# Kernel optimization log

Measured on AMD Instinct MI355X. Metric: run time of the kernel, lower is better.

Reference implementation:

```python
import jax, jax.numpy as jnp
import numpy as np

H = 8          # num_heads
SPARSITY = 0.1


def setup_inputs() -> dict:
    key = jax.random.key(0)
    ks = jax.random.split(key, 16)
    B, S, D = 2, 2048, 1024
    g2 = H * H  # 64, distill width
    std = 0.02
    inp = {
        "x":   jax.random.normal(ks[0], (B, S, D), dtype=jnp.float32),
        "Wq":  jax.random.normal(ks[1], (D, D)) * std, "bq": jnp.zeros((D,)),
        "Wk":  jax.random.normal(ks[2], (D, D)) * std, "bk": jnp.zeros((D,)),
        "Wv":  jax.random.normal(ks[3], (D, D)) * std, "bv": jnp.zeros((D,)),
        "Wo":  jax.random.normal(ks[4], (D, D)) * std, "bo": jnp.zeros((D,)),
        "Wd":  jax.random.normal(ks[5], (g2, g2)) * std, "bd": jnp.zeros((g2,)),
        "Wg":  jax.random.normal(ks[6], (g2, D)) * std,  "bg": jnp.zeros((g2,)),
        "Wgp": jax.random.normal(ks[7], (D, g2)) * std,  "bgp": jnp.zeros((D,)),
    }
    return inp


def reference(x, Wq, bq, Wk, bk, Wv, bv, Wo, bo, Wd, bd, Wg, bg, Wgp, bgp):
    B, S, D = x.shape
    Dh = D // H
    scale = Dh ** -0.5
    k = max(int(S * SPARSITY), 1)

    def heads(W, b):  # [B,S,D] -> [B,H,S,Dh]
        return (x @ W.T + b).reshape(B, S, H, Dh).transpose(0, 2, 1, 3)

    Q, K, V = heads(Wq, bq), heads(Wk, bk), heads(Wv, bv)

    scores = jnp.einsum("bhqd,bhkd->bhqk", Q, K) * scale       # [B,H,S,S]
    # per-row top-k threshold (k-th largest value of each query row)
    thr = jax.lax.top_k(scores, k)[0][..., k - 1:k]              # [B,H,S,1]
    masked = jnp.where(scores >= thr, scores, -jnp.inf)
    probs = jax.nn.softmax(masked, axis=-1)
    attn = jnp.einsum("bhqk,bhkd->bhqd", probs, V)               # [B,H,S,Dh]
    attn = attn.transpose(0, 2, 1, 3).reshape(B, S, D)           # [B,S,D]

    g2 = H * H
    distilled = (attn.reshape(-1, g2) @ Wd.T + bd).reshape(B, S, D)

    gate = jax.nn.sigmoid(x.mean(axis=1) @ Wg.T + bg)            # [B,g2]
    gate = (gate @ Wgp.T + bgp)[:, None, :]                      # [B,1,D]

    mixed = gate * distilled + (1.0 - gate) * attn
    return mixed @ Wo.T + bo
```

## Files before the change

kernel.cpp:

```cpp
#include <hip/hip_runtime.h>

typedef __attribute__((ext_vector_type(8))) short bf16x8;
typedef __attribute__((ext_vector_type(4))) float f32x4;
typedef __attribute__((ext_vector_type(4))) unsigned int u32x4;

#define DEVINL __device__ __forceinline__

DEVINL unsigned short f2bf(float f){
  unsigned int u = __float_as_uint(f);
  unsigned int r = (u + 0x7FFFu + ((u >> 16) & 1u)) >> 16;
  return (unsigned short)r;
}
DEVINL float bf2f(unsigned short h){ return __uint_as_float(((unsigned int)h) << 16); }
DEVINL unsigned int fkey(float f){
  unsigned int u = __float_as_uint(f);
  return (u & 0x80000000u) ? ~u : (u | 0x80000000u);
}
DEVINL float fkeyinv(unsigned int k){
  unsigned int u = (k & 0x80000000u) ? (k & 0x7FFFFFFFu) : ~k;
  return __uint_as_float(u);
}
DEVINL unsigned int cvtpk(float lo, float hi){
  unsigned int r;
  asm("v_cvt_pk_bf16_f32 %0, %1, %2" : "=v"(r) : "v"(lo), "v"(hi));
  return r;
}
DEVINL void gload16(void* lds, const void* g){
  __builtin_amdgcn_global_load_lds((const __attribute__((address_space(1))) void*)g,
                                   (__attribute__((address_space(3))) void*)lds, 16, 0, 0);
}

__global__ void prep_split_kernel(const float* __restrict__ src,
                                  unsigned short* __restrict__ hi,
                                  unsigned short* __restrict__ lo, int n){
  int i = blockIdx.x * 256 + threadIdx.x;
  if (i >= n) return;
  float f = src[i];
  unsigned short h = f2bf(f);
  hi[i] = h;
  if (lo) lo[i] = f2bf(f - bf2f(h));
}

template<bool SPLIT, int EPI>
__global__ __launch_bounds__(256) void gemm_kernel(
    const unsigned short* __restrict__ Ah, const unsigned short* __restrict__ Al,
    const unsigned short* __restrict__ Bh, const unsigned short* __restrict__ Bl,
    const float* __restrict__ bias0, const float* __restrict__ bias1, const float* __restrict__ bias2,
    unsigned short* __restrict__ qh, unsigned short* __restrict__ ql,
    unsigned short* __restrict__ kh, unsigned short* __restrict__ kl,
    unsigned short* __restrict__ vT, float* __restrict__ outf)
{
  const int K = 1024;
  __shared__ __align__(16) unsigned short sAh[128*32];
  __shared__ __align__(16) unsigned short sBh[128*32];
  __shared__ __align__(16) unsigned short sAl[SPLIT ? 128*32 : 8];
  __shared__ __align__(16) unsigned short sBl[SPLIT ? 128*32 : 8];

  const int tid = threadIdx.x;
  const int lane = tid & 63;
  const int w = tid >> 6;
  const int wr = w >> 1, wc = w & 1;
  const int l16 = lane & 15, lg = lane >> 4;
  const int bm = blockIdx.x, bn = blockIdx.y;

  const int srow = (lane >> 2);
  const int scol = (lane & 3) * 8;
  const int r0 = w * 32;

  f32x4 acc[4][4];
  #pragma unroll
  for (int i = 0; i < 4; i++)
    #pragma unroll
    for (int j = 0; j < 4; j++)
      acc[i][j] = (f32x4){0.f,0.f,0.f,0.f};

  for (int kt = 0; kt < K/32; ++kt){
    __syncthreads();
    #pragma unroll
    for (int cc = 0; cc < 2; cc++){
      const int rr = r0 + cc*16 + srow;
      const int lb = (r0 + cc*16) * 32;
      gload16(&sAh[lb], &Ah[(size_t)(bm*128 + rr)*K + kt*32 + scol]);
      gload16(&sBh[lb], &Bh[(size_t)(bn*128 + rr)*K + kt*32 + scol]);
      if constexpr (SPLIT){
        gload16(&sAl[lb], &Al[(size_t)(bm*128 + rr)*K + kt*32 + scol]);
        gload16(&sBl[lb], &Bl[(size_t)(bn*128 + rr)*K + kt*32 + scol]);
      }
    }
    __syncthreads();

    bf16x8 afh[4], afl[4], bfh[4], bfl[4];
    #pragma unroll
    for (int mi = 0; mi < 4; mi++){
      int off = (wr*64 + mi*16 + l16)*32 + lg*8;
      afh[mi] = *(const bf16x8*)&sAh[off];
      if constexpr (SPLIT) afl[mi] = *(const bf16x8*)&sAl[off];
    }
    #pragma unroll
    for (int ni = 0; ni < 4; ni++){
      int off = (wc*64 + ni*16 + l16)*32 + lg*8;
      bfh[ni] = *(const bf16x8*)&sBh[off];
      if constexpr (SPLIT) bfl[ni] = *(const bf16x8*)&sBl[off];
    }
    #pragma unroll
    for (int mi = 0; mi < 4; mi++)
      #pragma unroll
      for (int ni = 0; ni < 4; ni++){
        acc[mi][ni] = __builtin_amdgcn_mfma_f32_16x16x32_bf16(afh[mi], bfh[ni], acc[mi][ni], 0, 0, 0);
        if constexpr (SPLIT){
          acc[mi][ni] = __builtin_amdgcn_mfma_f32_16x16x32_bf16(afh[mi], bfl[ni], acc[mi][ni], 0, 0, 0);
          acc[mi][ni] = __builtin_amdgcn_mfma_f32_16x16x32_bf16(afl[mi], bfh[ni], acc[mi][ni], 0, 0, 0);
        }
      }
  }

  if constexpr (EPI == 0){
    const int wsel = (bn * 128) >> 10;
    const float* bias = (wsel == 0) ? bias0 : (wsel == 1) ? bias1 : bias2;
    #pragma unroll
    for (int mi = 0; mi < 4; mi++)
      #pragma unroll
      for (int ni = 0; ni < 4; ni++)
        #pragma unroll
        for (int i = 0; i < 4; i++){
          int m = bm*128 + wr*64 + mi*16 + lg*4 + i;
          int ng = bn*128 + wc*64 + ni*16 + l16;
          int n = ng & 1023;
          float v = acc[mi][ni][i] + bias[n];
          int b = m >> 11, s = m & 2047;
          int h = n >> 7, dh = n & 127;
          size_t base = (size_t)(b*8 + h)*262144;
          if (wsel == 2){
            size_t off = base + (size_t)(s>>5)*4096 + (dh>>4)*512
                       + (size_t)((((s>>3)&3)*16 + (dh&15))*8 + (s&7));
            vT[off] = f2bf(v);
          } else {
            size_t off = base + (size_t)(s>>4)*2048 + (dh>>5)*512
                       + (size_t)((((dh>>3)&3)*16 + (s&15))*8 + (dh&7));
            unsigned short hv = f2bf(v);
            if (wsel == 0){ qh[off] = hv; ql[off] = f2bf(v - bf2f(hv)); }
            else          { kh[off] = hv; kl[off] = f2bf(v - bf2f(hv)); }
          }
        }
  } else {
    #pragma unroll
    for (int mi = 0; mi < 4; mi++)
      #pragma unroll
      for (int ni = 0; ni < 4; ni++)
        #pragma unroll
        for (int i = 0; i < 4; i++){
          int m = bm*128 + wr*64 + mi*16 + lg*4 + i;
          int n = bn*128 + wc*64 + ni*16 + l16;
          outf[(size_t)m*1024 + n] = acc[mi][ni][i] + bias0[n];
        }
  }
}

__global__ __launch_bounds__(512, 4) void attn_kernel(
    const unsigned short* __restrict__ qh, const unsigned short* __restrict__ ql,
    const unsigned short* __restrict__ kh, const unsigned short* __restrict__ kl,
    const unsigned short* __restrict__ vT, float* __restrict__ attn_out)
{
  __shared__ __align__(16) float red[8][16][132];
  __shared__ float rpartm[8][16], rpartd[8][16];
  __shared__ unsigned int prefixv[16], kremv[16];
  unsigned int* hist = (unsigned int*)red;

  const int tid = threadIdx.x;
  const int lane = tid & 63;
  const int w = tid >> 6;
  const int l16 = lane & 15, lg = lane >> 4;
  const int swz = (blockIdx.x & 7) * 256 + (blockIdx.x >> 3);
  const int bh = swz >> 7, qb = swz & 127;
  const float scale = 0.08838834764831845f;

  const size_t base = (size_t)bh*262144;

  const size_t qpb = base + (size_t)qb*2048 + lane*8;
  bf16x8 aqh[4], aql[4];
  #pragma unroll
  for (int kk = 0; kk < 4; kk++){
    aqh[kk] = *(const bf16x8*)&qh[qpb + kk*512];
    aql[kk] = *(const bf16x8*)&ql[qpb + kk*512];
  }

  f32x4 acc[16];
  #pragma unroll
  for (int nt = 0; nt < 16; nt++){
    f32x4 a0 = (f32x4){0.f,0.f,0.f,0.f};
    f32x4 a1 = (f32x4){0.f,0.f,0.f,0.f};
    const size_t kb = base + (size_t)(w*16 + nt)*2048 + lane*8;
    __builtin_amdgcn_s_setprio(1);
    #pragma unroll
    for (int kk = 0; kk < 4; kk++){
      bf16x8 kbh = *(const bf16x8*)&kh[kb + kk*512];
      bf16x8 kbl = *(const bf16x8*)&kl[kb + kk*512];
      a0 = __builtin_amdgcn_mfma_f32_16x16x32_bf16(kbh, aqh[kk], a0, 0, 0, 0);
      a1 = __builtin_amdgcn_mfma_f32_16x16x32_bf16(kbh, aql[kk], a1, 0, 0, 0);
      a1 = __builtin_amdgcn_mfma_f32_16x16x32_bf16(kbl, aqh[kk], a1, 0, 0, 0);
    }
    __builtin_amdgcn_s_setprio(0);
    #pragma unroll
    for (int i = 0; i < 4; i++) acc[nt][i] = (a0[i] + a1[i]) * scale;
  }

  {
    float rm = -3.4e38f;
    #pragma unroll
    for (int nt = 0; nt < 16; nt++)
      #pragma unroll
      for (int i = 0; i < 4; i++) rm = fmaxf(rm, acc[nt][i]);
    rm = fmaxf(rm, __shfl_xor(rm, 16, 64));
    rm = fmaxf(rm, __shfl_xor(rm, 32, 64));
    if (lane < 16) rpartm[w][lane] = rm;
  }
  if (tid < 16){ prefixv[tid] = 0u; kremv[tid] = 204u; }

  #pragma unroll
  for (int nt = 0; nt < 16; nt++)
    #pragma unroll
    for (int i = 0; i < 4; i++)
      acc[nt][i] = __uint_as_float(fkey(acc[nt][i]));

  const int hco = (w >> 1) * (16*257);
  for (int pass = 3; pass >= 0; pass--){
    const int shift = pass*8;
    __syncthreads();
    for (int j = tid; j < 4*16*257; j += 512) hist[j] = 0u;
    __syncthreads();
    const unsigned int pf = prefixv[l16];
    const unsigned int mhi = (pass == 3) ? 0u : (0xFFFFFFFFu << (shift + 8));
    #pragma unroll
    for (int nt = 0; nt < 16; nt++)
      #pragma unroll
      for (int i = 0; i < 4; i++){
        unsigned int u = __float_as_uint(acc[nt][i]);
        if ((u & mhi) == pf)
          atomicAdd(&hist[hco + l16*257 + ((u >> shift) & 255u)], 1u);
      }
    __syncthreads();
    #pragma unroll
    for (int rr = 0; rr < 2; rr++){
      int r = w*2 + rr;
      unsigned int krem = kremv[r];
      unsigned int pfx  = prefixv[r];
      unsigned int cl[4], s4 = 0;
      #pragma unroll
      for (int t = 0; t < 4; t++){
        int idx = r*257 + 255 - 4*lane - t;
        cl[t] = hist[idx] + hist[16*257 + idx] + hist[2*16*257 + idx] + hist[3*16*257 + idx];
        s4 += cl[t];
      }
      unsigned int inc = s4;
      #pragma unroll
      for (int off = 1; off < 64; off <<= 1){
        unsigned int v = __shfl_up((int)inc, off, 64);
        if (lane >= off) inc += v;
      }
      unsigned int cb = inc - s4;
      #pragma unroll
      for (int t = 0; t < 4; t++){
        if (krem > cb && krem <= cb + cl[t]){
          int d = 255 - 4*lane - t;
          prefixv[r] = pfx | ((unsigned int)d << shift);
          kremv[r]   = krem - cb;
        }
        cb += cl[t];
      }
    }
  }
  __syncthreads();

  const unsigned int th = prefixv[l16];
  float rmax = rpartm[0][l16];
  #pragma unroll
  for (int w8 = 1; w8 < 8; w8++) rmax = fmaxf(rmax, rpartm[w8][l16]);
  const int src01 = ((lg & 1) << 5) + l16;
  const int src23 = src01 + 16;
  const size_t vb0 = base + (size_t)(w*8)*4096 + lane*8;
  float dn = 0.f;
  f32x4 pacc[8];
  #pragma unroll
  for (int dt = 0; dt < 8; dt++) pacc[dt] = (f32x4){0.f,0.f,0.f,0.f};
  #pragma unroll
  for (int t = 0; t < 8; t++){
    float p[8];
    #pragma unroll
    for (int j = 0; j < 4; j++){
      unsigned int u = __float_as_uint(acc[2*t][j]);
      p[j] = (u >= th) ? __expf(fkeyinv(u) - rmax) : 0.f;
    }
    #pragma unroll
    for (int j = 0; j < 4; j++){
      unsigned int u = __float_as_uint(acc[2*t+1][j]);
      p[4+j] = (u >= th) ? __expf(fkeyinv(u) - rmax) : 0.f;
    }
    unsigned int d0 = cvtpk(p[0], p[1]), d1 = cvtpk(p[2], p[3]);
    unsigned int d2 = cvtpk(p[4], p[5]), d3 = cvtpk(p[6], p[7]);
    dn += __uint_as_float(d0 << 16) + __uint_as_float(d0 & 0xFFFF0000u)
        + __uint_as_float(d1 << 16) + __uint_as_float(d1 & 0xFFFF0000u)
        + __uint_as_float(d2 << 16) + __uint_as_float(d2 & 0xFFFF0000u)
        + __uint_as_float(d3 << 16) + __uint_as_float(d3 & 0xFFFF0000u);
    unsigned int A0 = (unsigned int)__shfl((int)d0, src01, 64);
    unsigned int A1 = (unsigned int)__shfl((int)d1, src01, 64);
    unsigned int A2 = (unsigned int)__shfl((int)d0, src23, 64);
    unsigned int A3 = (unsigned int)__shfl((int)d1, src23, 64);
    unsigned int B0 = (unsigned int)__shfl((int)d2, src01, 64);
    unsigned int B1 = (unsigned int)__shfl((int)d3, src01, 64);
    unsigned int B2 = (unsigned int)__shfl((int)d2, src23, 64);
    unsigned int B3 = (unsigned int)__shfl((int)d3, src23, 64);
    u32x4 pdv = (lg < 2) ? (u32x4){A0, A1, A2, A3} : (u32x4){B0, B1, B2, B3};
    bf16x8 pa = __builtin_bit_cast(bf16x8, pdv);
    __builtin_amdgcn_s_setprio(1);
    #pragma unroll
    for (int dt = 0; dt < 8; dt++){
      bf16x8 bv = *(const bf16x8*)&vT[vb0 + (size_t)t*4096 + dt*512];
      pacc[dt] = __builtin_amdgcn_mfma_f32_16x16x32_bf16(pa, bv, pacc[dt], 0, 0, 0);
    }
    __builtin_amdgcn_s_setprio(0);
  }
  dn += __shfl_xor(dn, 16, 64);
  dn += __shfl_xor(dn, 32, 64);
  if (lane < 16) rpartd[w][lane] = dn;

  #pragma unroll
  for (int dt = 0; dt < 8; dt++)
    #pragma unroll
    for (int i = 0; i < 4; i++)
      red[w][lg*4 + i][dt*16 + l16] = pacc[dt][i];
  __syncthreads();

  {
    const int q = tid >> 5;
    const int c0 = (tid & 31) * 4;
    f32x4 s0 = (f32x4){0.f,0.f,0.f,0.f};
    #pragma unroll
    for (int w8 = 0; w8 < 8; w8++)
      s0 += *(const f32x4*)&red[w8][q][c0];
    float dnm = 0.f;
    #pragma unroll
    for (int w8 = 0; w8 < 8; w8++) dnm += rpartd[w8][q];
    const int b = bh >> 3, h = bh & 7;
    float* op = &attn_out[((size_t)b*2048 + qb*16 + q)*1024 + h*128 + c0];
    f32x4 o0;
    #pragma unroll
    for (int i = 0; i < 4; i++) o0[i] = s0[i] / dnm;
    *(f32x4*)op = o0;
  }
}

__global__ void mean_partial_kernel(const float* __restrict__ x, float* __restrict__ partial){
  int b = blockIdx.x >> 7, ch = blockIdx.x & 127;
  int tid = threadIdx.x;
  #pragma unroll
  for (int dc = 0; dc < 4; dc++){
    int d = dc*256 + tid;
    float s = 0.f;
    for (int ss = 0; ss < 16; ss++) s += x[((size_t)b*2048 + ch*16 + ss)*1024 + d];
    partial[((size_t)b*128 + ch)*1024 + d] = s;
  }
}

__global__ __launch_bounds__(512) void gate_sig_kernel(const float* __restrict__ partial,
    const float* __restrict__ Wg, const float* __restrict__ bg, float* __restrict__ gsig){
  __shared__ float xm[1024];
  const int b = blockIdx.x;
  const int tid = threadIdx.x, lane = tid & 63, w = tid >> 6;
  for (int d = tid; d < 1024; d += 512){
    float s = 0.f;
    for (int c = 0; c < 128; c++) s += partial[((size_t)b*128 + c)*1024 + d];
    xm[d] = s * (1.f/2048.f);
  }
  __syncthreads();
  for (int jj = 0; jj < 8; jj++){
    const int j = w*8 + jj;
    float s = 0.f;
    #pragma unroll
    for (int c = 0; c < 4; c++){
      f32x4 wv = *(const f32x4*)&Wg[(size_t)j*1024 + lane*16 + c*4];
      s += wv[0]*xm[lane*16 + c*4] + wv[1]*xm[lane*16 + c*4 + 1]
         + wv[2]*xm[lane*16 + c*4 + 2] + wv[3]*xm[lane*16 + c*4 + 3];
    }
    #pragma unroll
    for (int off = 1; off < 64; off <<= 1) s += __shfl_xor(s, off, 64);
    if (lane == 0) gsig[b*64 + j] = 1.f / (1.f + __expf(-(s + bg[j])));
  }
}

__global__ __launch_bounds__(256) void gate_proj_kernel(const float* __restrict__ gsig,
    const float* __restrict__ Wgp, const float* __restrict__ bgp, float* __restrict__ gate){
  __shared__ float gb[64];
  const int blk = blockIdx.x;
  const int b = blk >> 2;
  const int d = (blk & 3) * 256 + threadIdx.x;
  if (threadIdx.x < 64) gb[threadIdx.x] = gsig[b*64 + threadIdx.x];
  __syncthreads();
  float s = bgp[d];
  #pragma unroll
  for (int j4 = 0; j4 < 16; j4++){
    f32x4 wv = *(const f32x4*)&Wgp[(size_t)d*64 + j4*4];
    s += wv[0]*gb[j4*4] + wv[1]*gb[j4*4+1] + wv[2]*gb[j4*4+2] + wv[3]*gb[j4*4+3];
  }
  gate[b*1024 + d] = s;
}

__global__ __launch_bounds__(256) void mix_kernel(const float* __restrict__ attn,
    const float* __restrict__ Wd, const float* __restrict__ bd,
    const float* __restrict__ gate,
    unsigned short* __restrict__ mixedh, unsigned short* __restrict__ mixedl){
  __shared__ float sWdT[64*64];
  __shared__ float arow[1024];
  int tid = threadIdx.x;
  for (int i = tid; i < 4096; i += 256){
    int m = i >> 6, cc = i & 63;
    sWdT[i] = Wd[cc*64 + m];
  }
  int rbase = blockIdx.x * 16;
  for (int rr = 0; rr < 16; rr++){
    int row = rbase + rr;
    __syncthreads();
    for (int i = tid; i < 1024; i += 256) arow[i] = attn[(size_t)row*1024 + i];
    __syncthreads();
    int b = row >> 11;
    #pragma unroll
    for (int c4 = 0; c4 < 4; c4++){
      int dcol = c4*256 + tid;
      int j = dcol >> 6, cc = dcol & 63;
      float y = bd[cc];
      for (int m = 0; m < 64; m++) y += arow[j*64 + m] * sWdT[m*64 + cc];
      float g = gate[b*1024 + dcol];
      float mv = g*y + (1.f - g)*arow[dcol];
      unsigned short hv = f2bf(mv);
      mixedh[(size_t)row*1024 + dcol] = hv;
      mixedl[(size_t)row*1024 + dcol] = f2bf(mv - bf2f(hv));
    }
  }
}

extern "C" void kernel_launch(void* const* d_in, const int* in_sizes, int n_in,
                              void* d_out, int out_size, void* d_ws, size_t ws_size,
                              hipStream_t stream){
  (void)in_sizes; (void)n_in; (void)out_size; (void)ws_size;
  const float* x   = (const float*)d_in[0];
  const float* Wq  = (const float*)d_in[1];
  const float* bq  = (const float*)d_in[2];
  const float* Wk  = (const float*)d_in[3];
  const float* bk  = (const float*)d_in[4];
  const float* Wv  = (const float*)d_in[5];
  const float* bv  = (const float*)d_in[6];
  const float* Wo  = (const float*)d_in[7];
  const float* bo  = (const float*)d_in[8];
  const float* Wd  = (const float*)d_in[9];
  const float* bd  = (const float*)d_in[10];
  const float* Wg  = (const float*)d_in[11];
  const float* bg  = (const float*)d_in[12];
  const float* Wgp = (const float*)d_in[13];
  const float* bgp = (const float*)d_in[14];
  float* out = (float*)d_out;

  const size_t MiB = 1048576;
  char* ws = (char*)d_ws;
  unsigned short* xh     = (unsigned short*)(ws + 0*MiB);
  unsigned short* xl     = (unsigned short*)(ws + 8*MiB);
  float*          attnws = (float*)(ws + 0*MiB);
  unsigned short* whi    = (unsigned short*)(ws + 16*MiB);
  unsigned short* wlo    = (unsigned short*)(ws + 22*MiB);
  unsigned short* wohi   = (unsigned short*)(ws + 16*MiB);
  unsigned short* wolo   = (unsigned short*)(ws + 18*MiB);
  float*          partial= (float*)(ws + 20*MiB);
  float*          gatews = (float*)(ws + 21*MiB);
  float*          gsig   = (float*)(ws + 21*MiB + 16384);
  unsigned short* qh_    = (unsigned short*)(ws + 28*MiB);
  unsigned short* ql_    = (unsigned short*)(ws + 36*MiB);
  unsigned short* mixedh = (unsigned short*)(ws + 28*MiB);
  unsigned short* mixedl = (unsigned short*)(ws + 36*MiB);
  unsigned short* kh_    = (unsigned short*)(ws + 44*MiB);
  unsigned short* kl_    = (unsigned short*)(ws + 52*MiB);
  unsigned short* vT_    = (unsigned short*)(ws + 60*MiB);

  prep_split_kernel<<<16384, 256, 0, stream>>>(x,  xh, xl, 4194304);
  prep_split_kernel<<<4096,  256, 0, stream>>>(Wq, whi,           wlo,           1048576);
  prep_split_kernel<<<4096,  256, 0, stream>>>(Wk, whi + 1048576, wlo + 1048576, 1048576);
  prep_split_kernel<<<4096,  256, 0, stream>>>(Wv, whi + 2097152, wlo + 2097152, 1048576);

  gemm_kernel<true, 0><<<dim3(32, 24), 256, 0, stream>>>(
      xh, xl, whi, wlo, bq, bk, bv, qh_, ql_, kh_, kl_, vT_, nullptr);

  prep_split_kernel<<<4096,  256, 0, stream>>>(Wo, wohi, wolo, 1048576);

  attn_kernel<<<2048, 512, 0, stream>>>(qh_, ql_, kh_, kl_, vT_, attnws);

  mean_partial_kernel<<<256, 256, 0, stream>>>(x, partial);
  gate_sig_kernel<<<2, 512, 0, stream>>>(partial, Wg, bg, gsig);
  gate_proj_kernel<<<8, 256, 0, stream>>>(gsig, Wgp, bgp, gatews);

  mix_kernel<<<256, 256, 0, stream>>>(attnws, Wd, bd, gatews, mixedh, mixedl);

  gemm_kernel<true, 1><<<dim3(32, 8), 256, 0, stream>>>(
      mixedh, mixedl, wohi, wolo, bo, nullptr, nullptr,
      nullptr, nullptr, nullptr, nullptr, nullptr, out);
}
```

Baseline: 473.8 us.

## Fuse distill/gate mixing into attention epilogue and merge prep and gate kernels

Folds the 64x64 distill projection, gate blending and bf16 hi/lo split into the attention kernel's epilogue, so the fp32 attention output no longer makes a round trip through global memory and the separate mix kernel is gone. The gate computation is reordered to run before attention. The x/Wq/Wk/Wv split kernels are merged into one launch, and the two gate kernels are merged into one. This adds epilogue work and global Wd reads per attention block, plus an extra barrier, which may lengthen the attention kernel's tail.

```diff
diff --git a/kernel.cpp b/kernel.cpp
--- a/kernel.cpp
+++ b/kernel.cpp
@@ -28,6 +28,27 @@
 DEVINL void gload16(void* lds, const void* g){
   __builtin_amdgcn_global_load_lds((const __attribute__((address_space(1))) void*)g,
                                    (__attribute__((address_space(3))) void*)lds, 16, 0, 0);
+}
+
+__global__ void prep_all_kernel(const float* __restrict__ x,
+                                const float* __restrict__ Wq, const float* __restrict__ Wk,
+                                const float* __restrict__ Wv,
+                                unsigned short* __restrict__ xh, unsigned short* __restrict__ xl,
+                                unsigned short* __restrict__ whi, unsigned short* __restrict__ wlo){
+  const int NX = 4194304, NW = 1048576;
+  int i = blockIdx.x * 256 + threadIdx.x;
+  if (i < NX){
+    float f = x[i];
+    unsigned short h = f2bf(f);
+    xh[i] = h; xl[i] = f2bf(f - bf2f(h));
+  } else {
+    int j = i - NX;
+    const float* W = (j < NW) ? Wq : (j < 2*NW) ? Wk : Wv;
+    int o = (j < NW) ? j : (j < 2*NW) ? (j - NW) : (j - 2*NW);
+    float f = W[o];
+    unsigned short h = f2bf(f);
+    whi[j] = h; wlo[j] = f2bf(f - bf2f(h));
+  }
 }
 
 __global__ void prep_split_kernel(const float* __restrict__ src,
@@ -159,7 +180,9 @@
 __global__ __launch_bounds__(512, 4) void attn_kernel(
     const unsigned short* __restrict__ qh, const unsigned short* __restrict__ ql,
     const unsigned short* __restrict__ kh, const unsigned short* __restrict__ kl,
-    const unsigned short* __restrict__ vT, float* __restrict__ attn_out)
+    const unsigned short* __restrict__ vT,
+    const float* __restrict__ Wd, const float* __restrict__ bd, const float* __restrict__ gate,
+    unsigned short* __restrict__ mixedh, unsigned short* __restrict__ mixedl)
 {
   __shared__ __align__(16) float red[8][16][132];
   __shared__ float rpartm[8][16], rpartd[8][16];
@@ -331,7 +354,7 @@
   __syncthreads();
 
   {
-    const int q = tid >> 5;
+    const int q  = tid >> 5;
     const int c0 = (tid & 31) * 4;
     f32x4 s0 = (f32x4){0.f,0.f,0.f,0.f};
     #pragma unroll
@@ -340,12 +363,38 @@
     float dnm = 0.f;
     #pragma unroll
     for (int w8 = 0; w8 < 8; w8++) dnm += rpartd[w8][q];
+    f32x4 o;
+    #pragma unroll
+    for (int i = 0; i < 4; i++) o[i] = s0[i] / dnm;
+    *(f32x4*)&red[0][q][c0] = o;
+    __syncthreads();
+
     const int b = bh >> 3, h = bh & 7;
-    float* op = &attn_out[((size_t)b*2048 + qb*16 + q)*1024 + h*128 + c0];
-    f32x4 o0;
-    #pragma unroll
-    for (int i = 0; i < 4; i++) o0[i] = s0[i] / dnm;
-    *(f32x4*)op = o0;
+    const int j64 = c0 & 64;
+    const int ccb = c0 & 63;
+    f32x4 y = (f32x4){bd[ccb], bd[ccb+1], bd[ccb+2], bd[ccb+3]};
+    #pragma unroll
+    for (int m4 = 0; m4 < 16; m4++){
+      f32x4 ov = *(const f32x4*)&red[0][q][j64 + m4*4];
+      #pragma unroll
+      for (int i = 0; i < 4; i++){
+        f32x4 wv = *(const f32x4*)&Wd[(size_t)(ccb + i)*64 + m4*4];
+        y[i] += ov[0]*wv[0];
+        y[i] += ov[1]*wv[1];
+        y[i] += ov[2]*wv[2];
+        y[i] += ov[3]*wv[3];
+      }
+    }
+    const int col = h*128 + c0;
+    const size_t row = (size_t)b*2048 + qb*16 + q;
+    #pragma unroll
+    for (int i = 0; i < 4; i++){
+      float g  = gate[b*1024 + col + i];
+      float mv = g*y[i] + (1.f - g)*o[i];
+      unsigned short hv = f2bf(mv);
+      mixedh[row*1024 + col + i] = hv;
+      mixedl[row*1024 + col + i] = f2bf(mv - bf2f(hv));
+    }
   }
 }
 
@@ -361,9 +410,11 @@
   }
 }
 
-__global__ __launch_bounds__(512) void gate_sig_kernel(const float* __restrict__ partial,
-    const float* __restrict__ Wg, const float* __restrict__ bg, float* __restrict__ gsig){
+__global__ __launch_bounds__(512) void gate_kernel2(const float* __restrict__ partial,
+    const float* __restrict__ Wg, const float* __restrict__ bg,
+    const float* __restrict__ Wgp, const float* __restrict__ bgp, float* __restrict__ gate){
   __shared__ float xm[1024];
+  __shared__ float gb[64];
   const int b = blockIdx.x;
   const int tid = threadIdx.x, lane = tid & 63, w = tid >> 6;
   for (int d = tid; d < 1024; d += 512){
@@ -383,57 +434,17 @@
     }
     #pragma unroll
     for (int off = 1; off < 64; off <<= 1) s += __shfl_xor(s, off, 64);
-    if (lane == 0) gsig[b*64 + j] = 1.f / (1.f + __expf(-(s + bg[j])));
-  }
-}
-
-__global__ __launch_bounds__(256) void gate_proj_kernel(const float* __restrict__ gsig,
-    const float* __restrict__ Wgp, const float* __restrict__ bgp, float* __restrict__ gate){
-  __shared__ float gb[64];
-  const int blk = blockIdx.x;
-  const int b = blk >> 2;
-  const int d = (blk & 3) * 256 + threadIdx.x;
-  if (threadIdx.x < 64) gb[threadIdx.x] = gsig[b*64 + threadIdx.x];
+    if (lane == 0) gb[j] = 1.f / (1.f + __expf(-(s + bg[j])));
+  }
   __syncthreads();
-  float s = bgp[d];
-  #pragma unroll
-  for (int j4 = 0; j4 < 16; j4++){
-    f32x4 wv = *(const f32x4*)&Wgp[(size_t)d*64 + j4*4];
-    s += wv[0]*gb[j4*4] + wv[1]*gb[j4*4+1] + wv[2]*gb[j4*4+2] + wv[3]*gb[j4*4+3];
-  }
-  gate[b*1024 + d] = s;
-}
-
-__global__ __launch_bounds__(256) void mix_kernel(const float* __restrict__ attn,
-    const float* __restrict__ Wd, const float* __restrict__ bd,
-    const float* __restrict__ gate,
-    unsigned short* __restrict__ mixedh, unsigned short* __restrict__ mixedl){
-  __shared__ float sWdT[64*64];
-  __shared__ float arow[1024];
-  int tid = threadIdx.x;
-  for (int i = tid; i < 4096; i += 256){
-    int m = i >> 6, cc = i & 63;
-    sWdT[i] = Wd[cc*64 + m];
-  }
-  int rbase = blockIdx.x * 16;
-  for (int rr = 0; rr < 16; rr++){
-    int row = rbase + rr;
-    __syncthreads();
-    for (int i = tid; i < 1024; i += 256) arow[i] = attn[(size_t)row*1024 + i];
-    __syncthreads();
-    int b = row >> 11;
-    #pragma unroll
-    for (int c4 = 0; c4 < 4; c4++){
-      int dcol = c4*256 + tid;
-      int j = dcol >> 6, cc = dcol & 63;
-      float y = bd[cc];
-      for (int m = 0; m < 64; m++) y += arow[j*64 + m] * sWdT[m*64 + cc];
-      float g = gate[b*1024 + dcol];
-      float mv = g*y + (1.f - g)*arow[dcol];
-      unsigned short hv = f2bf(mv);
-      mixedh[(size_t)row*1024 + dcol] = hv;
-      mixedl[(size_t)row*1024 + dcol] = f2bf(mv - bf2f(hv));
-    }
+  for (int d = tid; d < 1024; d += 512){
+    float s = bgp[d];
+    #pragma unroll
+    for (int j4 = 0; j4 < 16; j4++){
+      f32x4 wv = *(const f32x4*)&Wgp[(size_t)d*64 + j4*4];
+      s += wv[0]*gb[j4*4] + wv[1]*gb[j4*4+1] + wv[2]*gb[j4*4+2] + wv[3]*gb[j4*4+3];
+    }
+    gate[b*1024 + d] = s;
   }
 }
 
@@ -462,39 +473,31 @@
   char* ws = (char*)d_ws;
   unsigned short* xh     = (unsigned short*)(ws + 0*MiB);
   unsigned short* xl     = (unsigned short*)(ws + 8*MiB);
-  float*          attnws = (float*)(ws + 0*MiB);
+  unsigned short* mixedh = (unsigned short*)(ws + 0*MiB);
+  unsigned short* mixedl = (unsigned short*)(ws + 8*MiB);
   unsigned short* whi    = (unsigned short*)(ws + 16*MiB);
   unsigned short* wlo    = (unsigned short*)(ws + 22*MiB);
   unsigned short* wohi   = (unsigned short*)(ws + 16*MiB);
   unsigned short* wolo   = (unsigned short*)(ws + 18*MiB);
   float*          partial= (float*)(ws + 20*MiB);
   float*          gatews = (float*)(ws + 21*MiB);
-  float*          gsig   = (float*)(ws + 21*MiB + 16384);
   unsigned short* qh_    = (unsigned short*)(ws + 28*MiB);
   unsigned short* ql_    = (unsigned short*)(ws + 36*MiB);
-  unsigned short* mixedh = (unsigned short*)(ws + 28*MiB);
-  unsigned short* mixedl = (unsigned short*)(ws + 36*MiB);
   unsigned short* kh_    = (unsigned short*)(ws + 44*MiB);
   unsigned short* kl_    = (unsigned short*)(ws + 52*MiB);
   unsigned short* vT_    = (unsigned short*)(ws + 60*MiB);
 
-  prep_split_kernel<<<16384, 256, 0, stream>>>(x,  xh, xl, 4194304);
-  prep_split_kernel<<<4096,  256, 0, stream>>>(Wq, whi,           wlo,           1048576);
-  prep_split_kernel<<<4096,  256, 0, stream>>>(Wk, whi + 1048576, wlo + 1048576, 1048576);
-  prep_split_kernel<<<4096,  256, 0, stream>>>(Wv, whi + 2097152, wlo + 2097152, 1048576);
+  prep_all_kernel<<<28672, 256, 0, stream>>>(x, Wq, Wk, Wv, xh, xl, whi, wlo);
 
   gemm_kernel<true, 0><<<dim3(32, 24), 256, 0, stream>>>(
       xh, xl, whi, wlo, bq, bk, bv, qh_, ql_, kh_, kl_, vT_, nullptr);
 
-  prep_split_kernel<<<4096,  256, 0, stream>>>(Wo, wohi, wolo, 1048576);
-
-  attn_kernel<<<2048, 512, 0, stream>>>(qh_, ql_, kh_, kl_, vT_, attnws);
-
+  prep_split_kernel<<<4096, 256, 0, stream>>>(Wo, wohi, wolo, 1048576);
   mean_partial_kernel<<<256, 256, 0, stream>>>(x, partial);
-  gate_sig_kernel<<<2, 512, 0, stream>>>(partial, Wg, bg, gsig);
-  gate_proj_kernel<<<8, 256, 0, stream>>>(gsig, Wgp, bgp, gatews);
-
-  mix_kernel<<<256, 256, 0, stream>>>(attnws, Wd, bd, gatews, mixedh, mixedl);
+  gate_kernel2<<<2, 512, 0, stream>>>(partial, Wg, bg, Wgp, bgp, gatews);
+
+  attn_kernel<<<2048, 512, 0, stream>>>(qh_, ql_, kh_, kl_, vT_,
+                                        Wd, bd, gatews, mixedh, mixedl);
 
   gemm_kernel<true, 1><<<dim3(32, 8), 256, 0, stream>>>(
       mixedh, mixedl, wohi, wolo, bo, nullptr, nullptr,
```

Result: slower. 537.6 us (+13.5%).
